# Kernel optimization log

Measured on AMD Instinct MI355X. Metric: run time of the kernel, lower is better.

## Reference

```python
import jax, jax.numpy as jnp
import numpy as np

LN_EPS = 1e-5
MASK_FILL = -1e9


def setup_inputs() -> dict:
    key = jax.random.key(0)
    ks = jax.random.split(key, 8)
    B, S, D = 32, 1024, 1280
    Dout = 1280
    emb = jax.random.normal(ks[0], (B, S, D), dtype=jnp.float32)
    mask = jnp.ones((B, S), dtype=jnp.int32)
    w = 0.02
    return {
        "embeddings": emb,
        "attention_mask": mask,
        "Wq": jax.random.normal(ks[1], (D, D), jnp.float32) * w,
        "bq": jnp.zeros((D,), jnp.float32),
        "Wk": jax.random.normal(ks[2], (D, D), jnp.float32) * w,
        "bk": jnp.zeros((D,), jnp.float32),
        "Wv": jax.random.normal(ks[3], (D, D), jnp.float32) * w,
        "bv": jnp.zeros((D,), jnp.float32),
        "Wo": jax.random.normal(ks[4], (Dout, D), jnp.float32) * w,
        "bo": jnp.zeros((Dout,), jnp.float32),
        "gamma": jnp.ones((Dout,), jnp.float32),
        "beta": jnp.zeros((Dout,), jnp.float32),
    }


def reference(embeddings, attention_mask, Wq, bq, Wk, bk, Wv, bv, Wo, bo, gamma, beta):
    # Original torch module computes full [B,S,S] self-attention but only
    # consumes context[:, 0, :]. Mathematically identical (same output and
    # same gradients) to computing attention for query row 0 only.
    B, S, D = embeddings.shape
    scale = D ** -0.5
    q0 = embeddings[:, 0, :] @ Wq.T + bq                      # [B, D]
    k = jnp.einsum("bsd,ed->bse", embeddings, Wk) + bk        # [B, S, D]
    v = jnp.einsum("bsd,ed->bse", embeddings, Wv) + bv        # [B, S, D]
    scores = jnp.einsum("bd,bsd->bs", q0, k) * scale          # [B, S]
    scores = jnp.where(attention_mask == 0, MASK_FILL, scores)
    weights = jax.nn.softmax(scores, axis=-1)                 # [B, S]
    ctx = jnp.einsum("bs,bsd->bd", weights, v)                # [B, D]
    # output projection: Linear -> LayerNorm -> ReLU (dropout = identity in eval)
    h = ctx @ Wo.T + bo                                       # [B, Dout]
    mu = jnp.mean(h, axis=-1, keepdims=True)
    var = jnp.mean(jnp.square(h - mu), axis=-1, keepdims=True)
    h = (h - mu) * jax.lax.rsqrt(var + LN_EPS) * gamma + beta
    return jax.nn.relu(h)
```

## Files before the change

kernel.cpp:

```cpp
#include <hip/hip_runtime.h>
#include <hip/hip_bf16.h>

constexpr int cB = 32;
constexpr int cS = 1024;
constexpr int cD = 1280;
constexpr int KC = 32;
constexpr int NKC = cD / KC;
constexpr int NNC = cD / 256;

#define LN_EPS 1e-5f
#define MASK_FILL -1e9f
#define SCALE 0.02795084971874737f

__global__ __launch_bounds__(256) void k_mmT_p1(const float* __restrict__ A,
                                                size_t lda,
                                                const float* __restrict__ W,
                                                float* __restrict__ part) {
    __shared__ float s_t[KC * 257];
    int t = threadIdx.x;
    int nc = blockIdx.x % NNC, kc = blockIdx.x / NNC;
    int n0 = nc * 256, k0 = kc * KC;

#pragma unroll
    for (int p = 0; p < 8; ++p) {
        int r  = (t >> 3) + p * 32;
        int ko = (t & 7) * 4;
        float4 wv = *reinterpret_cast<const float4*>(W + (size_t)(n0 + r) * cD + k0 + ko);
        s_t[(ko + 0) * 257 + r] = wv.x;
        s_t[(ko + 1) * 257 + r] = wv.y;
        s_t[(ko + 2) * 257 + r] = wv.z;
        s_t[(ko + 3) * 257 + r] = wv.w;
    }
    __syncthreads();

    float w[KC];
#pragma unroll
    for (int kk = 0; kk < KC; ++kk) w[kk] = s_t[kk * 257 + t];

#pragma unroll
    for (int b = 0; b < cB; ++b) {
        const float* Ab = A + (size_t)b * lda + k0;
        float a0 = 0.f, a1 = 0.f, a2 = 0.f, a3 = 0.f;
#pragma unroll
        for (int kk = 0; kk < KC; kk += 4) {
            a0 += Ab[kk + 0] * w[kk + 0];
            a1 += Ab[kk + 1] * w[kk + 1];
            a2 += Ab[kk + 2] * w[kk + 2];
            a3 += Ab[kk + 3] * w[kk + 3];
        }
        part[(size_t)kc * (cB * cD) + b * cD + n0 + t] = (a0 + a1) + (a2 + a3);
    }
}

__global__ __launch_bounds__(256) void k_mm_p1(const float* __restrict__ A,
                                               size_t lda,
                                               const float* __restrict__ B,
                                               float* __restrict__ part) {
    int t = threadIdx.x;
    int nc = blockIdx.x % NNC, kc = blockIdx.x / NNC;
    int n0 = nc * 256, k0 = kc * KC;

    float w[KC];
#pragma unroll
    for (int kk = 0; kk < KC; ++kk)
        w[kk] = B[(size_t)(k0 + kk) * cD + n0 + t];

#pragma unroll
    for (int b = 0; b < cB; ++b) {
        const float* Ab = A + (size_t)b * lda + k0;
        float a0 = 0.f, a1 = 0.f, a2 = 0.f, a3 = 0.f;
#pragma unroll
        for (int kk = 0; kk < KC; kk += 4) {
            a0 += Ab[kk + 0] * w[kk + 0];
            a1 += Ab[kk + 1] * w[kk + 1];
            a2 += Ab[kk + 2] * w[kk + 2];
            a3 += Ab[kk + 3] * w[kk + 3];
        }
        part[(size_t)kc * (cB * cD) + b * cD + n0 + t] = (a0 + a1) + (a2 + a3);
    }
}

__global__ __launch_bounds__(256) void k_mm_red(const float* __restrict__ part,
                                                const float* __restrict__ bias,
                                                float* __restrict__ out) {
    int i = blockIdx.x * 256 + threadIdx.x;
    float s = 0.f;
#pragma unroll
    for (int c = 0; c < NKC; ++c) s += part[(size_t)c * (cB * cD) + i];
    if (bias) s += bias[i % cD];
    out[i] = s;
}

__global__ __launch_bounds__(256) void k_qb(const float* __restrict__ q0,
                                            const float* __restrict__ bk,
                                            float* __restrict__ qb) {
    int w = threadIdx.x >> 6, lane = threadIdx.x & 63;
    int d0 = lane * 4;
    float4 bkr[5];
#pragma unroll
    for (int it = 0; it < 5; ++it)
        bkr[it] = *reinterpret_cast<const float4*>(bk + it * 256 + d0);
#pragma unroll
    for (int r = 0; r < 8; ++r) {
        int b = w * 8 + r;
        float dot = 0.f;
#pragma unroll
        for (int it = 0; it < 5; ++it) {
            float4 qv = *reinterpret_cast<const float4*>(q0 + b * cD + it * 256 + d0);
            dot += qv.x * bkr[it].x + qv.y * bkr[it].y + qv.z * bkr[it].z + qv.w * bkr[it].w;
        }
#pragma unroll
        for (int off = 32; off; off >>= 1) dot += __shfl_xor(dot, off, 64);
        if (lane == 0) qb[b] = dot;
    }
}

__global__ __launch_bounds__(256) void k_attn(const float* __restrict__ emb,
                                              const float* __restrict__ qk,
                                              const float* __restrict__ qb,
                                              const int* __restrict__ mask,
                                              float* __restrict__ pm,
                                              float* __restrict__ pl,
                                              float* __restrict__ pacc) {
    int blk = blockIdx.x;
    int b = blk >> 5, sc = blk & 31;
    int w = threadIdx.x >> 6, lane = threadIdx.x & 63;
    int d0 = lane * 4;

    float4 qkr[5];
#pragma unroll
    for (int it = 0; it < 5; ++it)
        qkr[it] = *reinterpret_cast<const float4*>(qk + b * cD + it * 256 + d0);
    float qbv = qb[b];

    float m = -INFINITY, l = 0.f;
    float4 acc[5];
#pragma unroll
    for (int it = 0; it < 5; ++it) acc[it] = make_float4(0.f, 0.f, 0.f, 0.f);

    int s0 = sc * 32 + w * 8;
    for (int r = 0; r < 8; ++r) {
        int s = s0 + r;
        const float* e = emb + (size_t)(b * cS + s) * cD + d0;
        float4 er[5];
#pragma unroll
        for (int it = 0; it < 5; ++it)
            er[it] = *reinterpret_cast<const float4*>(e + it * 256);
        float dot = 0.f;
#pragma unroll
        for (int it = 0; it < 5; ++it)
            dot += er[it].x * qkr[it].x + er[it].y * qkr[it].y
                 + er[it].z * qkr[it].z + er[it].w * qkr[it].w;
#pragma unroll
        for (int off = 32; off; off >>= 1) dot += __shfl_xor(dot, off, 64);
        float scv = (mask[b * cS + s] == 0) ? MASK_FILL : (dot + qbv) * SCALE;
        if (scv > m) {
            float f = __expf(m - scv);
            l *= f;
#pragma unroll
            for (int it = 0; it < 5; ++it) {
                acc[it].x *= f; acc[it].y *= f; acc[it].z *= f; acc[it].w *= f;
            }
            m = scv;
        }
        float p = __expf(scv - m);
        l += p;
#pragma unroll
        for (int it = 0; it < 5; ++it) {
            acc[it].x += p * er[it].x; acc[it].y += p * er[it].y;
            acc[it].z += p * er[it].z; acc[it].w += p * er[it].w;
        }
    }

    __shared__ float s_m[4], s_l[4];
    __shared__ float s_acc[cD];
    if (lane == 0) { s_m[w] = m; s_l[w] = l; }
    __syncthreads();
    float M = fmaxf(fmaxf(s_m[0], s_m[1]), fmaxf(s_m[2], s_m[3]));
    float f = __expf(m - M);
    if (w == 0) {
#pragma unroll
        for (int it = 0; it < 5; ++it)
            *reinterpret_cast<float4*>(s_acc + it * 256 + d0) =
                make_float4(acc[it].x * f, acc[it].y * f, acc[it].z * f, acc[it].w * f);
    }
    __syncthreads();
    if (w == 1) {
#pragma unroll
        for (int it = 0; it < 5; ++it) {
            float4* p4 = reinterpret_cast<float4*>(s_acc + it * 256 + d0);
            float4 v = *p4;
            *p4 = make_float4(v.x + acc[it].x * f, v.y + acc[it].y * f,
                              v.z + acc[it].z * f, v.w + acc[it].w * f);
        }
    }
    __syncthreads();
    if (w == 2) {
#pragma unroll
        for (int it = 0; it < 5; ++it) {
            float4* p4 = reinterpret_cast<float4*>(s_acc + it * 256 + d0);
            float4 v = *p4;
            *p4 = make_float4(v.x + acc[it].x * f, v.y + acc[it].y * f,
                              v.z + acc[it].z * f, v.w + acc[it].w * f);
        }
    }
    __syncthreads();
    if (w == 3) {
#pragma unroll
        for (int it = 0; it < 5; ++it) {
            float4* p4 = reinterpret_cast<float4*>(s_acc + it * 256 + d0);
            float4 v = *p4;
            *p4 = make_float4(v.x + acc[it].x * f, v.y + acc[it].y * f,
                              v.z + acc[it].z * f, v.w + acc[it].w * f);
        }
    }
    __syncthreads();

    if (threadIdx.x == 0) {
        float lt = s_l[0] * __expf(s_m[0] - M) + s_l[1] * __expf(s_m[1] - M)
                 + s_l[2] * __expf(s_m[2] - M) + s_l[3] * __expf(s_m[3] - M);
        pm[blk] = M; pl[blk] = lt;
    }
#pragma unroll
    for (int j = 0; j < 5; ++j)
        pacc[(size_t)blk * cD + threadIdx.x + 256 * j] = s_acc[threadIdx.x + 256 * j];
}

__global__ __launch_bounds__(256) void k_attn_red(const float* __restrict__ pm,
                                                  const float* __restrict__ pl,
                                                  const float* __restrict__ pacc,
                                                  float* __restrict__ ectx) {
    int b = blockIdx.x / 5, j = blockIdx.x % 5;
    int d = j * 256 + threadIdx.x;
    float M = -INFINITY;
    for (int i = 0; i < 32; ++i) M = fmaxf(M, pm[b * 32 + i]);
    float L = 0.f, a = 0.f;
    for (int i = 0; i < 32; ++i) {
        float wf = __expf(pm[b * 32 + i] - M);
        L += pl[b * 32 + i] * wf;
        a += wf * pacc[(size_t)(b * 32 + i) * cD + d];
    }
    ectx[b * cD + d] = a / L;
}

__global__ __launch_bounds__(256) void k_ln(const float* __restrict__ h,
                                            const float* __restrict__ gamma,
                                            const float* __restrict__ beta,
                                            float* __restrict__ out) {
    int b = blockIdx.x;
    __shared__ float red[8];
    int wid = threadIdx.x >> 6, lane = threadIdx.x & 63;
    float v[5];
    float sum = 0.f;
#pragma unroll
    for (int j = 0; j < 5; ++j) {
        v[j] = h[b * cD + threadIdx.x + 256 * j];
        sum += v[j];
    }
#pragma unroll
    for (int off = 32; off; off >>= 1) sum += __shfl_xor(sum, off, 64);
    if (lane == 0) red[wid] = sum;
    __syncthreads();
    float mu = (red[0] + red[1] + red[2] + red[3]) * (1.f / cD);
    float vs = 0.f;
#pragma unroll
    for (int j = 0; j < 5; ++j) { float t = v[j] - mu; vs += t * t; }
#pragma unroll
    for (int off = 32; off; off >>= 1) vs += __shfl_xor(vs, off, 64);
    if (lane == 0) red[4 + wid] = vs;
    __syncthreads();
    float var = (red[4] + red[5] + red[6] + red[7]) * (1.f / cD);
    float inv = rsqrtf(var + LN_EPS);
#pragma unroll
    for (int j = 0; j < 5; ++j) {
        int idx = threadIdx.x + 256 * j;
        float o = (v[j] - mu) * inv * gamma[idx] + beta[idx];
        out[b * cD + idx] = fmaxf(o, 0.f);
    }
}

extern "C" void kernel_launch(void* const* d_in, const int* in_sizes, int n_in,
                              void* d_out, int out_size, void* d_ws, size_t ws_size,
                              hipStream_t stream) {
    const float* emb   = (const float*)d_in[0];
    const int*   mask  = (const int*)d_in[1];
    const float* Wq    = (const float*)d_in[2];
    const float* bq    = (const float*)d_in[3];
    const float* Wk    = (const float*)d_in[4];
    const float* bk    = (const float*)d_in[5];
    const float* Wv    = (const float*)d_in[6];
    const float* bv    = (const float*)d_in[7];
    const float* Wo    = (const float*)d_in[8];
    const float* bo    = (const float*)d_in[9];
    const float* gamma = (const float*)d_in[10];
    const float* beta  = (const float*)d_in[11];

    float* ws   = (float*)d_ws;
    float* part = ws;
    float* q0   = part + NKC * cB * cD;
    float* qk   = q0 + cB * cD;
    float* qb   = qk + cB * cD;
    float* pm   = qb + cB;
    float* pl   = pm + 1024;
    float* pacc = pl + 1024;
    float* ectx = pacc + (size_t)1024 * cD;
    float* ctx  = ectx + cB * cD;
    float* h    = ctx + cB * cD;

    const int mmGrid  = NNC * NKC;
    const int redGrid = cB * cD / 256;

    k_mmT_p1<<<mmGrid, 256, 0, stream>>>(emb, (size_t)cS * cD, Wq, part);
    k_mm_red<<<redGrid, 256, 0, stream>>>(part, bq, q0);
    k_qb<<<1, 256, 0, stream>>>(q0, bk, qb);
    k_mm_p1<<<mmGrid, 256, 0, stream>>>(q0, (size_t)cD, Wk, part);
    k_mm_red<<<redGrid, 256, 0, stream>>>(part, nullptr, qk);
    k_attn<<<cB * 32, 256, 0, stream>>>(emb, qk, qb, mask, pm, pl, pacc);
    k_attn_red<<<redGrid, 256, 0, stream>>>(pm, pl, pacc, ectx);
    k_mmT_p1<<<mmGrid, 256, 0, stream>>>(ectx, (size_t)cD, Wv, part);
    k_mm_red<<<redGrid, 256, 0, stream>>>(part, bv, ctx);
    k_mmT_p1<<<mmGrid, 256, 0, stream>>>(ctx, (size_t)cD, Wo, part);
    k_mm_red<<<redGrid, 256, 0, stream>>>(part, bo, h);
    k_ln<<<cB, 256, 0, stream>>>(h, gamma, beta, (float*)d_out);
}
```

Baseline: 354.8 us.

## Replace split-K partial buffers and reduce kernels with atomic accumulation

Split-K GEMM blocks now atomically add into bias-preinitialized outputs instead of writing partial buffers that separate reduction kernels sum. The q·bk bias term is computed inside the attention kernel, removing the k_qb launch. The serialized per-wave shared-memory merge in attention becomes a parallel sum over per-wave buffers. This cuts launches and partial-buffer traffic, at the cost of atomic contention and a nondeterministic summation order.

```diff
diff --git a/kernel.cpp b/kernel.cpp
--- a/kernel.cpp
+++ b/kernel.cpp
@@ -12,10 +12,25 @@
 #define MASK_FILL -1e9f
 #define SCALE 0.02795084971874737f
 
-__global__ __launch_bounds__(256) void k_mmT_p1(const float* __restrict__ A,
-                                                size_t lda,
-                                                const float* __restrict__ W,
-                                                float* __restrict__ part) {
+__global__ __launch_bounds__(256) void k_init(const float* __restrict__ bq,
+                                              const float* __restrict__ bv,
+                                              const float* __restrict__ bo,
+                                              float* __restrict__ q0,
+                                              float* __restrict__ qk,
+                                              float* __restrict__ ctx,
+                                              float* __restrict__ h) {
+    int i = blockIdx.x * 256 + threadIdx.x;
+    int n = i % cD;
+    q0[i]  = bq[n];
+    qk[i]  = 0.f;
+    ctx[i] = bv[n];
+    h[i]   = bo[n];
+}
+
+__global__ __launch_bounds__(256) void k_mmT_p1a(const float* __restrict__ A,
+                                                 size_t lda,
+                                                 const float* __restrict__ W,
+                                                 float* __restrict__ out) {
     __shared__ float s_t[KC * 257];
     int t = threadIdx.x;
     int nc = blockIdx.x % NNC, kc = blockIdx.x / NNC;
@@ -48,14 +63,14 @@
             a2 += Ab[kk + 2] * w[kk + 2];
             a3 += Ab[kk + 3] * w[kk + 3];
         }
-        part[(size_t)kc * (cB * cD) + b * cD + n0 + t] = (a0 + a1) + (a2 + a3);
-    }
-}
-
-__global__ __launch_bounds__(256) void k_mm_p1(const float* __restrict__ A,
-                                               size_t lda,
-                                               const float* __restrict__ B,
-                                               float* __restrict__ part) {
+        atomicAdd(&out[b * cD + n0 + t], (a0 + a1) + (a2 + a3));
+    }
+}
+
+__global__ __launch_bounds__(256) void k_mm_p1a(const float* __restrict__ A,
+                                                size_t lda,
+                                                const float* __restrict__ B,
+                                                float* __restrict__ out) {
     int t = threadIdx.x;
     int nc = blockIdx.x % NNC, kc = blockIdx.x / NNC;
     int n0 = nc * 256, k0 = kc * KC;
@@ -76,62 +91,39 @@
             a2 += Ab[kk + 2] * w[kk + 2];
             a3 += Ab[kk + 3] * w[kk + 3];
         }
-        part[(size_t)kc * (cB * cD) + b * cD + n0 + t] = (a0 + a1) + (a2 + a3);
-    }
-}
-
-__global__ __launch_bounds__(256) void k_mm_red(const float* __restrict__ part,
-                                                const float* __restrict__ bias,
-                                                float* __restrict__ out) {
-    int i = blockIdx.x * 256 + threadIdx.x;
-    float s = 0.f;
-#pragma unroll
-    for (int c = 0; c < NKC; ++c) s += part[(size_t)c * (cB * cD) + i];
-    if (bias) s += bias[i % cD];
-    out[i] = s;
-}
-
-__global__ __launch_bounds__(256) void k_qb(const float* __restrict__ q0,
-                                            const float* __restrict__ bk,
-                                            float* __restrict__ qb) {
-    int w = threadIdx.x >> 6, lane = threadIdx.x & 63;
-    int d0 = lane * 4;
-    float4 bkr[5];
-#pragma unroll
-    for (int it = 0; it < 5; ++it)
-        bkr[it] = *reinterpret_cast<const float4*>(bk + it * 256 + d0);
-#pragma unroll
-    for (int r = 0; r < 8; ++r) {
-        int b = w * 8 + r;
-        float dot = 0.f;
-#pragma unroll
-        for (int it = 0; it < 5; ++it) {
-            float4 qv = *reinterpret_cast<const float4*>(q0 + b * cD + it * 256 + d0);
-            dot += qv.x * bkr[it].x + qv.y * bkr[it].y + qv.z * bkr[it].z + qv.w * bkr[it].w;
-        }
-#pragma unroll
-        for (int off = 32; off; off >>= 1) dot += __shfl_xor(dot, off, 64);
-        if (lane == 0) qb[b] = dot;
+        atomicAdd(&out[b * cD + n0 + t], (a0 + a1) + (a2 + a3));
     }
 }
 
 __global__ __launch_bounds__(256) void k_attn(const float* __restrict__ emb,
                                               const float* __restrict__ qk,
-                                              const float* __restrict__ qb,
+                                              const float* __restrict__ q0,
+                                              const float* __restrict__ bk,
                                               const int* __restrict__ mask,
                                               float* __restrict__ pm,
                                               float* __restrict__ pl,
                                               float* __restrict__ pacc) {
+    __shared__ float s_all[4][cD];
+    __shared__ float s_m[4], s_l[4], s_qb[4];
     int blk = blockIdx.x;
     int b = blk >> 5, sc = blk & 31;
     int w = threadIdx.x >> 6, lane = threadIdx.x & 63;
     int d0 = lane * 4;
 
+    float pq = 0.f;
+#pragma unroll
+    for (int j = 0; j < 5; ++j)
+        pq += q0[b * cD + j * 256 + threadIdx.x] * bk[j * 256 + threadIdx.x];
+#pragma unroll
+    for (int off = 32; off; off >>= 1) pq += __shfl_xor(pq, off, 64);
+    if (lane == 0) s_qb[w] = pq;
+
     float4 qkr[5];
 #pragma unroll
     for (int it = 0; it < 5; ++it)
         qkr[it] = *reinterpret_cast<const float4*>(qk + b * cD + it * 256 + d0);
-    float qbv = qb[b];
+    __syncthreads();
+    float qbv = s_qb[0] + s_qb[1] + s_qb[2] + s_qb[3];
 
     float m = -INFINITY, l = 0.f;
     float4 acc[5];
@@ -172,48 +164,14 @@
         }
     }
 
-    __shared__ float s_m[4], s_l[4];
-    __shared__ float s_acc[cD];
     if (lane == 0) { s_m[w] = m; s_l[w] = l; }
     __syncthreads();
     float M = fmaxf(fmaxf(s_m[0], s_m[1]), fmaxf(s_m[2], s_m[3]));
     float f = __expf(m - M);
-    if (w == 0) {
-#pragma unroll
-        for (int it = 0; it < 5; ++it)
-            *reinterpret_cast<float4*>(s_acc + it * 256 + d0) =
-                make_float4(acc[it].x * f, acc[it].y * f, acc[it].z * f, acc[it].w * f);
-    }
-    __syncthreads();
-    if (w == 1) {
-#pragma unroll
-        for (int it = 0; it < 5; ++it) {
-            float4* p4 = reinterpret_cast<float4*>(s_acc + it * 256 + d0);
-            float4 v = *p4;
-            *p4 = make_float4(v.x + acc[it].x * f, v.y + acc[it].y * f,
-                              v.z + acc[it].z * f, v.w + acc[it].w * f);
-        }
-    }
-    __syncthreads();
-    if (w == 2) {
-#pragma unroll
-        for (int it = 0; it < 5; ++it) {
-            float4* p4 = reinterpret_cast<float4*>(s_acc + it * 256 + d0);
-            float4 v = *p4;
-            *p4 = make_float4(v.x + acc[it].x * f, v.y + acc[it].y * f,
-                              v.z + acc[it].z * f, v.w + acc[it].w * f);
-        }
-    }
-    __syncthreads();
-    if (w == 3) {
-#pragma unroll
-        for (int it = 0; it < 5; ++it) {
-            float4* p4 = reinterpret_cast<float4*>(s_acc + it * 256 + d0);
-            float4 v = *p4;
-            *p4 = make_float4(v.x + acc[it].x * f, v.y + acc[it].y * f,
-                              v.z + acc[it].z * f, v.w + acc[it].w * f);
-        }
-    }
+#pragma unroll
+    for (int it = 0; it < 5; ++it)
+        *reinterpret_cast<float4*>(&s_all[w][it * 256 + d0]) =
+            make_float4(acc[it].x * f, acc[it].y * f, acc[it].z * f, acc[it].w * f);
     __syncthreads();
 
     if (threadIdx.x == 0) {
@@ -222,8 +180,11 @@
         pm[blk] = M; pl[blk] = lt;
     }
 #pragma unroll
-    for (int j = 0; j < 5; ++j)
-        pacc[(size_t)blk * cD + threadIdx.x + 256 * j] = s_acc[threadIdx.x + 256 * j];
+    for (int j = 0; j < 5; ++j) {
+        int d = j * 256 + threadIdx.x;
+        pacc[(size_t)blk * cD + d] =
+            s_all[0][d] + s_all[1][d] + s_all[2][d] + s_all[3][d];
+    }
 }
 
 __global__ __launch_bounds__(256) void k_attn_red(const float* __restrict__ pm,
@@ -296,30 +257,24 @@
     const float* beta  = (const float*)d_in[11];
 
     float* ws   = (float*)d_ws;
-    float* part = ws;
-    float* q0   = part + NKC * cB * cD;
+    float* q0   = ws;
     float* qk   = q0 + cB * cD;
-    float* qb   = qk + cB * cD;
-    float* pm   = qb + cB;
+    float* ctx  = qk + cB * cD;
+    float* h    = ctx + cB * cD;
+    float* pm   = h + cB * cD;
     float* pl   = pm + 1024;
     float* pacc = pl + 1024;
     float* ectx = pacc + (size_t)1024 * cD;
-    float* ctx  = ectx + cB * cD;
-    float* h    = ctx + cB * cD;
 
     const int mmGrid  = NNC * NKC;
     const int redGrid = cB * cD / 256;
 
-    k_mmT_p1<<<mmGrid, 256, 0, stream>>>(emb, (size_t)cS * cD, Wq, part);
-    k_mm_red<<<redGrid, 256, 0, stream>>>(part, bq, q0);
-    k_qb<<<1, 256, 0, stream>>>(q0, bk, qb);
-    k_mm_p1<<<mmGrid, 256, 0, stream>>>(q0, (size_t)cD, Wk, part);
-    k_mm_red<<<redGrid, 256, 0, stream>>>(part, nullptr, qk);
-    k_attn<<<cB * 32, 256, 0, stream>>>(emb, qk, qb, mask, pm, pl, pacc);
+    k_init<<<redGrid, 256, 0, stream>>>(bq, bv, bo, q0, qk, ctx, h);
+    k_mmT_p1a<<<mmGrid, 256, 0, stream>>>(emb, (size_t)cS * cD, Wq, q0);
+    k_mm_p1a<<<mmGrid, 256, 0, stream>>>(q0, (size_t)cD, Wk, qk);
+    k_attn<<<cB * 32, 256, 0, stream>>>(emb, qk, q0, bk, mask, pm, pl, pacc);
     k_attn_red<<<redGrid, 256, 0, stream>>>(pm, pl, pacc, ectx);
-    k_mmT_p1<<<mmGrid, 256, 0, stream>>>(ectx, (size_t)cD, Wv, part);
-    k_mm_red<<<redGrid, 256, 0, stream>>>(part, bv, ctx);
-    k_mmT_p1<<<mmGrid, 256, 0, stream>>>(ctx, (size_t)cD, Wo, part);
-    k_mm_red<<<redGrid, 256, 0, stream>>>(part, bo, h);
+    k_mmT_p1a<<<mmGrid, 256, 0, stream>>>(ectx, (size_t)cD, Wv, ctx);
+    k_mmT_p1a<<<mmGrid, 256, 0, stream>>>(ctx, (size_t)cD, Wo, h);
     k_ln<<<cB, 256, 0, stream>>>(h, gamma, beta, (float*)d_out);
 }
```

Result: slower. 363.8 us (+2.5%).

## Replace split-K transposed GEMVs with warp-per-output dot kernels and fuse reductions

Applied to the files above, without the earlier changes.

The three transposed matrix-vector projections (Wq, Wv, Wo) become a single-pass kernel where each wavefront computes one output column for 16 batch rows with a shuffle reduction, folding in the bias. This removes the split-K partial buffer writes and the separate reduction launches. The qb computation is merged into the qk reduction kernel, and the attention block's serialized per-warp shared-memory accumulation is replaced by parallel per-warp slots summed once. KC is halved for the remaining Wk split-K GEMM, trading more partials for more blocks.

```diff
diff --git a/kernel.cpp b/kernel.cpp
--- a/kernel.cpp
+++ b/kernel.cpp
@@ -4,7 +4,7 @@
 constexpr int cB = 32;
 constexpr int cS = 1024;
 constexpr int cD = 1280;
-constexpr int KC = 32;
+constexpr int KC = 16;
 constexpr int NKC = cD / KC;
 constexpr int NNC = cD / 256;
 
@@ -12,34 +12,57 @@
 #define MASK_FILL -1e9f
 #define SCALE 0.02795084971874737f
 
-__global__ __launch_bounds__(256) void k_mmT_p1(const float* __restrict__ A,
-                                                size_t lda,
-                                                const float* __restrict__ W,
-                                                float* __restrict__ part) {
-    __shared__ float s_t[KC * 257];
+__global__ __launch_bounds__(256) void k_dotT(const float* __restrict__ A,
+                                              size_t lda,
+                                              const float* __restrict__ W,
+                                              const float* __restrict__ bias,
+                                              float* __restrict__ out) {
+    int w = threadIdx.x >> 6, lane = threadIdx.x & 63;
+    int gw = blockIdx.x * 4 + w;
+    int n = gw >> 1;
+    int bh = (gw & 1) * 16;
+    int d0 = lane * 4;
+
+    float4 wr[5];
+#pragma unroll
+    for (int it = 0; it < 5; ++it)
+        wr[it] = *reinterpret_cast<const float4*>(W + (size_t)n * cD + it * 256 + d0);
+    float bn = bias[n];
+
+#pragma unroll
+    for (int bi = 0; bi < 16; ++bi) {
+        int b = bh + bi;
+        const float* a = A + (size_t)b * lda + d0;
+        float4 av[5];
+#pragma unroll
+        for (int it = 0; it < 5; ++it)
+            av[it] = *reinterpret_cast<const float4*>(a + it * 256);
+        float dot = 0.f;
+#pragma unroll
+        for (int it = 0; it < 5; ++it)
+            dot += av[it].x * wr[it].x + av[it].y * wr[it].y
+                 + av[it].z * wr[it].z + av[it].w * wr[it].w;
+#pragma unroll
+        for (int off = 32; off; off >>= 1) dot += __shfl_xor(dot, off, 64);
+        if (lane == 0) out[b * cD + n] = dot + bn;
+    }
+}
+
+__global__ __launch_bounds__(256) void k_mm_p1(const float* __restrict__ A,
+                                               const float* __restrict__ B,
+                                               float* __restrict__ part) {
     int t = threadIdx.x;
     int nc = blockIdx.x % NNC, kc = blockIdx.x / NNC;
     int n0 = nc * 256, k0 = kc * KC;
 
-#pragma unroll
-    for (int p = 0; p < 8; ++p) {
-        int r  = (t >> 3) + p * 32;
-        int ko = (t & 7) * 4;
-        float4 wv = *reinterpret_cast<const float4*>(W + (size_t)(n0 + r) * cD + k0 + ko);
-        s_t[(ko + 0) * 257 + r] = wv.x;
-        s_t[(ko + 1) * 257 + r] = wv.y;
-        s_t[(ko + 2) * 257 + r] = wv.z;
-        s_t[(ko + 3) * 257 + r] = wv.w;
-    }
-    __syncthreads();
-
     float w[KC];
 #pragma unroll
-    for (int kk = 0; kk < KC; ++kk) w[kk] = s_t[kk * 257 + t];
+    for (int kk = 0; kk < KC; ++kk)
+        w[kk] = B[(size_t)(k0 + kk) * cD + n0 + t];
 
 #pragma unroll
     for (int b = 0; b < cB; ++b) {
-        const float* Ab = A + (size_t)b * lda + k0;
+        const float* Ab = A + (size_t)b * cD + k0;
         float a0 = 0.f, a1 = 0.f, a2 = 0.f, a3 = 0.f;
 #pragma unroll
         for (int kk = 0; kk < KC; kk += 4) {
@@ -52,66 +75,38 @@
     }
 }
 
-__global__ __launch_bounds__(256) void k_mm_p1(const float* __restrict__ A,
-                                               size_t lda,
-                                               const float* __restrict__ B,
-                                               float* __restrict__ part) {
-    int t = threadIdx.x;
-    int nc = blockIdx.x % NNC, kc = blockIdx.x / NNC;
-    int n0 = nc * 256, k0 = kc * KC;
-
-    float w[KC];
-#pragma unroll
-    for (int kk = 0; kk < KC; ++kk)
-        w[kk] = B[(size_t)(k0 + kk) * cD + n0 + t];
-
-#pragma unroll
-    for (int b = 0; b < cB; ++b) {
-        const float* Ab = A + (size_t)b * lda + k0;
-        float a0 = 0.f, a1 = 0.f, a2 = 0.f, a3 = 0.f;
-#pragma unroll
-        for (int kk = 0; kk < KC; kk += 4) {
-            a0 += Ab[kk + 0] * w[kk + 0];
-            a1 += Ab[kk + 1] * w[kk + 1];
-            a2 += Ab[kk + 2] * w[kk + 2];
-            a3 += Ab[kk + 3] * w[kk + 3];
-        }
-        part[(size_t)kc * (cB * cD) + b * cD + n0 + t] = (a0 + a1) + (a2 + a3);
-    }
-}
-
-__global__ __launch_bounds__(256) void k_mm_red(const float* __restrict__ part,
-                                                const float* __restrict__ bias,
-                                                float* __restrict__ out) {
-    int i = blockIdx.x * 256 + threadIdx.x;
-    float s = 0.f;
-#pragma unroll
-    for (int c = 0; c < NKC; ++c) s += part[(size_t)c * (cB * cD) + i];
-    if (bias) s += bias[i % cD];
-    out[i] = s;
-}
-
-__global__ __launch_bounds__(256) void k_qb(const float* __restrict__ q0,
-                                            const float* __restrict__ bk,
-                                            float* __restrict__ qb) {
-    int w = threadIdx.x >> 6, lane = threadIdx.x & 63;
-    int d0 = lane * 4;
-    float4 bkr[5];
-#pragma unroll
-    for (int it = 0; it < 5; ++it)
-        bkr[it] = *reinterpret_cast<const float4*>(bk + it * 256 + d0);
-#pragma unroll
-    for (int r = 0; r < 8; ++r) {
-        int b = w * 8 + r;
-        float dot = 0.f;
-#pragma unroll
-        for (int it = 0; it < 5; ++it) {
-            float4 qv = *reinterpret_cast<const float4*>(q0 + b * cD + it * 256 + d0);
-            dot += qv.x * bkr[it].x + qv.y * bkr[it].y + qv.z * bkr[it].z + qv.w * bkr[it].w;
-        }
-#pragma unroll
-        for (int off = 32; off; off >>= 1) dot += __shfl_xor(dot, off, 64);
-        if (lane == 0) qb[b] = dot;
+__global__ __launch_bounds__(256) void k_mm_red_qb(const float* __restrict__ part,
+                                                   const float* __restrict__ q0,
+                                                   const float* __restrict__ bk,
+                                                   float* __restrict__ qk,
+                                                   float* __restrict__ qb) {
+    if (blockIdx.x < 160) {
+        int i = blockIdx.x * 256 + threadIdx.x;
+        float s = 0.f;
+#pragma unroll
+        for (int c = 0; c < NKC; ++c) s += part[(size_t)c * (cB * cD) + i];
+        qk[i] = s;
+    } else {
+        int w = threadIdx.x >> 6, lane = threadIdx.x & 63;
+        int d0 = lane * 4;
+        float4 bkr[5];
+#pragma unroll
+        for (int it = 0; it < 5; ++it)
+            bkr[it] = *reinterpret_cast<const float4*>(bk + it * 256 + d0);
+#pragma unroll
+        for (int r = 0; r < 8; ++r) {
+            int b = w * 8 + r;
+            float dot = 0.f;
+#pragma unroll
+            for (int it = 0; it < 5; ++it) {
+                float4 qv = *reinterpret_cast<const float4*>(q0 + b * cD + it * 256 + d0);
+                dot += qv.x * bkr[it].x + qv.y * bkr[it].y
+                     + qv.z * bkr[it].z + qv.w * bkr[it].w;
+            }
+#pragma unroll
+            for (int off = 32; off; off >>= 1) dot += __shfl_xor(dot, off, 64);
+            if (lane == 0) qb[b] = dot;
+        }
     }
 }
 
@@ -122,6 +117,8 @@
                                               float* __restrict__ pm,
                                               float* __restrict__ pl,
                                               float* __restrict__ pacc) {
+    __shared__ float s_all[4][cD];
+    __shared__ float s_m[4], s_l[4];
     int blk = blockIdx.x;
     int b = blk >> 5, sc = blk & 31;
     int w = threadIdx.x >> 6, lane = threadIdx.x & 63;
@@ -172,48 +169,14 @@
         }
     }
 
-    __shared__ float s_m[4], s_l[4];
-    __shared__ float s_acc[cD];
     if (lane == 0) { s_m[w] = m; s_l[w] = l; }
     __syncthreads();
     float M = fmaxf(fmaxf(s_m[0], s_m[1]), fmaxf(s_m[2], s_m[3]));
     float f = __expf(m - M);
-    if (w == 0) {
-#pragma unroll
-        for (int it = 0; it < 5; ++it)
-            *reinterpret_cast<float4*>(s_acc + it * 256 + d0) =
-                make_float4(acc[it].x * f, acc[it].y * f, acc[it].z * f, acc[it].w * f);
-    }
-    __syncthreads();
-    if (w == 1) {
-#pragma unroll
-        for (int it = 0; it < 5; ++it) {
-            float4* p4 = reinterpret_cast<float4*>(s_acc + it * 256 + d0);
-            float4 v = *p4;
-            *p4 = make_float4(v.x + acc[it].x * f, v.y + acc[it].y * f,
-                              v.z + acc[it].z * f, v.w + acc[it].w * f);
-        }
-    }
-    __syncthreads();
-    if (w == 2) {
-#pragma unroll
-        for (int it = 0; it < 5; ++it) {
-            float4* p4 = reinterpret_cast<float4*>(s_acc + it * 256 + d0);
-            float4 v = *p4;
-            *p4 = make_float4(v.x + acc[it].x * f, v.y + acc[it].y * f,
-                              v.z + acc[it].z * f, v.w + acc[it].w * f);
-        }
-    }
-    __syncthreads();
-    if (w == 3) {
-#pragma unroll
-        for (int it = 0; it < 5; ++it) {
-            float4* p4 = reinterpret_cast<float4*>(s_acc + it * 256 + d0);
-            float4 v = *p4;
-            *p4 = make_float4(v.x + acc[it].x * f, v.y + acc[it].y * f,
-                              v.z + acc[it].z * f, v.w + acc[it].w * f);
-        }
-    }
+#pragma unroll
+    for (int it = 0; it < 5; ++it)
+        *reinterpret_cast<float4*>(&s_all[w][it * 256 + d0]) =
+            make_float4(acc[it].x * f, acc[it].y * f, acc[it].z * f, acc[it].w * f);
     __syncthreads();
 
     if (threadIdx.x == 0) {
@@ -222,8 +185,11 @@
         pm[blk] = M; pl[blk] = lt;
     }
 #pragma unroll
-    for (int j = 0; j < 5; ++j)
-        pacc[(size_t)blk * cD + threadIdx.x + 256 * j] = s_acc[threadIdx.x + 256 * j];
+    for (int j = 0; j < 5; ++j) {
+        int d = j * 256 + threadIdx.x;
+        pacc[(size_t)blk * cD + d] =
+            s_all[0][d] + s_all[1][d] + s_all[2][d] + s_all[3][d];
+    }
 }
 
 __global__ __launch_bounds__(256) void k_attn_red(const float* __restrict__ pm,
@@ -307,19 +273,12 @@
     float* ctx  = ectx + cB * cD;
     float* h    = ctx + cB * cD;
 
-    const int mmGrid  = NNC * NKC;
-    const int redGrid = cB * cD / 256;
-
-    k_mmT_p1<<<mmGrid, 256, 0, stream>>>(emb, (size_t)cS * cD, Wq, part);
-    k_mm_red<<<redGrid, 256, 0, stream>>>(part, bq, q0);
-    k_qb<<<1, 256, 0, stream>>>(q0, bk, qb);
-    k_mm_p1<<<mmGrid, 256, 0, stream>>>(q0, (size_t)cD, Wk, part);
-    k_mm_red<<<redGrid, 256, 0, stream>>>(part, nullptr, qk);
+    k_dotT<<<640, 256, 0, stream>>>(emb, (size_t)cS * cD, Wq, bq, q0);
+    k_mm_p1<<<NNC * NKC, 256, 0, stream>>>(q0, Wk, part);
+    k_mm_red_qb<<<161, 256, 0, stream>>>(part, q0, bk, qk, qb);
     k_attn<<<cB * 32, 256, 0, stream>>>(emb, qk, qb, mask, pm, pl, pacc);
-    k_attn_red<<<redGrid, 256, 0, stream>>>(pm, pl, pacc, ectx);
-    k_mmT_p1<<<mmGrid, 256, 0, stream>>>(ectx, (size_t)cD, Wv, part);
-    k_mm_red<<<redGrid, 256, 0, stream>>>(part, bv, ctx);
-    k_mmT_p1<<<mmGrid, 256, 0, stream>>>(ctx, (size_t)cD, Wo, part);
-    k_mm_red<<<redGrid, 256, 0, stream>>>(part, bo, h);
+    k_attn_red<<<160, 256, 0, stream>>>(pm, pl, pacc, ectx);
+    k_dotT<<<640, 256, 0, stream>>>(ectx, (size_t)cD, Wv, bv, ctx);
+    k_dotT<<<640, 256, 0, stream>>>(ctx, (size_t)cD, Wo, bo, h);
     k_ln<<<cB, 256, 0, stream>>>(h, gamma, beta, (float*)d_out);
 }
```

After: 345.8 us. -2.5%, faster.
